# Kernel optimization log

Hardware: AMD Instinct MI355X
Metric: run time of the kernel (lower is better)

Reference implementation:

```python
import jax, jax.numpy as jnp
import numpy as np

B = 8388608  # batch of Euler-angle triples


def _euler_to_vec(angles):
    # angles: [B, 3] = (yaw, pitch, roll)
    # v = R_yaw @ R_pitch @ R_roll @ [0, 0, 1], expanded analytically:
    #   R_roll  @ e_z = [0, -sr, cr]
    #   R_pitch @ ... = [sp*cr, -sr, cp*cr]
    #   R_yaw   @ ... = [cy*sp*cr + sy*sr, sy*sp*cr - cy*sr, cp*cr]
    y, p, r = angles[:, 0], angles[:, 1], angles[:, 2]
    cy, sy = jnp.cos(y), jnp.sin(y)
    cp, sp = jnp.cos(p), jnp.sin(p)
    cr, sr = jnp.cos(r), jnp.sin(r)
    return jnp.stack([cy * sp * cr + sy * sr,
                      sy * sp * cr - cy * sr,
                      cp * cr], axis=-1)  # [B, 3]


def setup_inputs() -> dict:
    key = jax.random.key(0)
    k1, k2 = jax.random.split(key)
    output = jax.random.uniform(k1, (B, 3), dtype=jnp.float32)
    target = jax.random.uniform(k2, (B, 3), dtype=jnp.float32)
    return {"output": output, "target": target}


def reference(output, target):
    two_pi = 2.0 * jnp.pi
    out_ang = two_pi * (output - 0.5)
    tgt_ang = two_pi * (target - 0.5)
    vo = _euler_to_vec(out_ang)  # [B, 3]
    vt = _euler_to_vec(tgt_ang)  # [B, 3]
    cross = jnp.cross(vo, vt)                      # [B, 3]
    cross_norm = jnp.linalg.norm(cross, axis=-1)   # [B]
    dot = jnp.sum(vo * vt, axis=-1)                # [B]
    per_sample = 1.0 - cross_norm + dot
    return jnp.sum(per_sample)
```

## Files before the change

kernel.cpp:

```cpp
#include <hip/hip_runtime.h>
#include <math.h>


#define NBLOCKS 1024
#define NTHREADS 512
#define TILE_ROWS 1024
#define TILE_F2 (TILE_ROWS * 3 / 2)

__device__ __forceinline__ float2 ntload2(const double* p) {
  double d = __builtin_nontemporal_load(p);
  return __builtin_bit_cast(float2, d);
}

__device__ __forceinline__ float sample_loss(float a, float b, float c,
                                             float d, float e, float f) {
  float oy = a - 0.5f, op = b - 0.5f, orr = c - 0.5f;
  float ty = d - 0.5f, tp = e - 0.5f, trr = f - 0.5f;

  float cy = __builtin_amdgcn_cosf(oy), sy = __builtin_amdgcn_sinf(oy);
  float cp = __builtin_amdgcn_cosf(op), sp = __builtin_amdgcn_sinf(op);
  float cr = __builtin_amdgcn_cosf(orr), sr = __builtin_amdgcn_sinf(orr);

  float vox = cy * sp * cr + sy * sr;
  float voy = sy * sp * cr - cy * sr;
  float voz = cp * cr;

  float cy2 = __builtin_amdgcn_cosf(ty), sy2 = __builtin_amdgcn_sinf(ty);
  float cp2 = __builtin_amdgcn_cosf(tp), sp2 = __builtin_amdgcn_sinf(tp);
  float cr2 = __builtin_amdgcn_cosf(trr), sr2 = __builtin_amdgcn_sinf(trr);

  float vtx = cy2 * sp2 * cr2 + sy2 * sr2;
  float vty = sy2 * sp2 * cr2 - cy2 * sr2;
  float vtz = cp2 * cr2;

  float crx = voy * vtz - voz * vty;
  float cry = voz * vtx - vox * vtz;
  float crz = vox * vty - voy * vtx;

  float cn = sqrtf(crx * crx + cry * cry + crz * crz);
  float dot = vox * vtx + voy * vty + voz * vtz;
  return 1.0f - cn + dot;
}

template <int NT>
__device__ __forceinline__ float block_reduce(float acc) {
  #pragma unroll
  for (int off = 32; off > 0; off >>= 1) acc += __shfl_down(acc, off, 64);
  __shared__ float ws[NT / 64];
  int lane = threadIdx.x & 63;
  int wave = threadIdx.x >> 6;
  if (lane == 0) ws[wave] = acc;
  __syncthreads();
  float tot = 0.0f;
  if (threadIdx.x == 0) {
    #pragma unroll
    for (int w = 0; w < NT / 64; ++w) tot += ws[w];
  }
  return tot;
}

__global__ __launch_bounds__(NTHREADS) void loss_partial_kernel(
    const float* __restrict__ out, const float* __restrict__ tgt,
    float* __restrict__ partial, int B) {
  __shared__ float2 ldsO2[TILE_F2];
  __shared__ float2 ldsT2[TILE_F2];
  const float* ldsO = (const float*)ldsO2;
  const float* ldsT = (const float*)ldsT2;

  const double* __restrict__ o2 = (const double*)out;
  const double* __restrict__ t2 = (const double*)tgt;

  const int t = threadIdx.x;
  const int ntiles = B / TILE_ROWS;

  float acc = 0.0f;

  int tile = blockIdx.x;
  float2 a0, a1, a2, b0, b1, b2;
  if (tile < ntiles) {
    const int g = tile * TILE_F2 + t;
    a0 = ntload2(o2 + g); a1 = ntload2(o2 + g + NTHREADS); a2 = ntload2(o2 + g + 2 * NTHREADS);
    b0 = ntload2(t2 + g); b1 = ntload2(t2 + g + NTHREADS); b2 = ntload2(t2 + g + 2 * NTHREADS);
  }

  while (tile < ntiles) {
    ldsO2[t] = a0; ldsO2[t + NTHREADS] = a1; ldsO2[t + 2 * NTHREADS] = a2;
    ldsT2[t] = b0; ldsT2[t + NTHREADS] = b1; ldsT2[t + 2 * NTHREADS] = b2;
    __syncthreads();

    const int next = tile + gridDim.x;
    if (next < ntiles) {
      const int g = next * TILE_F2 + t;
      a0 = ntload2(o2 + g); a1 = ntload2(o2 + g + NTHREADS); a2 = ntload2(o2 + g + 2 * NTHREADS);
      b0 = ntload2(t2 + g); b1 = ntload2(t2 + g + NTHREADS); b2 = ntload2(t2 + g + 2 * NTHREADS);
    }

    #pragma unroll
    for (int k = 0; k < TILE_ROWS / NTHREADS; ++k) {
      const int r = t + k * NTHREADS;
      acc += sample_loss(ldsO[3 * r], ldsO[3 * r + 1], ldsO[3 * r + 2],
                         ldsT[3 * r], ldsT[3 * r + 1], ldsT[3 * r + 2]);
    }
    __syncthreads();
    tile = next;
  }

  const int done = ntiles * TILE_ROWS;
  for (int r = done + blockIdx.x * NTHREADS + t; r < B;
       r += gridDim.x * NTHREADS) {
    acc += sample_loss(out[3 * r], out[3 * r + 1], out[3 * r + 2],
                       tgt[3 * r], tgt[3 * r + 1], tgt[3 * r + 2]);
  }

  float tot = block_reduce<NTHREADS>(acc);
  if (t == 0) partial[blockIdx.x] = tot;
}

__global__ __launch_bounds__(64) void final_reduce_kernel(
    const float* __restrict__ partial, int n, float* __restrict__ out) {
  float acc = 0.0f;
  for (int i = threadIdx.x; i < n; i += 64) acc += partial[i];
  #pragma unroll
  for (int off = 32; off > 0; off >>= 1) acc += __shfl_down(acc, off, 64);
  if (threadIdx.x == 0) out[0] = acc;
}

extern "C" void kernel_launch(void* const* d_in, const int* in_sizes, int n_in,
                              void* d_out, int out_size, void* d_ws, size_t ws_size,
                              hipStream_t stream) {
  const float* d_output = (const float*)d_in[0];
  const float* d_target = (const float*)d_in[1];
  float* partial = (float*)d_ws;
  float* out = (float*)d_out;
  const int B = in_sizes[0] / 3;

  loss_partial_kernel<<<NBLOCKS, NTHREADS, 0, stream>>>(d_output, d_target,
                                                        partial, B);
  final_reduce_kernel<<<1, 64, 0, stream>>>(partial, NBLOCKS, out);
}
```

Measured before the change: 38.59 us.

## Stage tiles via global_load_lds with double-buffered LDS, double grid size

Replaces register-staged nontemporal loads plus LDS stores with direct global-to-LDS loads (12-byte per lane) into a double-buffered shared tile, and doubles the block count. This is meant to remove the register round-trip and the extra LDS write instructions, and to increase memory-level parallelism. The loop relies on the single __syncthreads to order the async LDS writes, with no explicit vmcnt wait, so correctness depends on the compiler inserting waits. LDS use doubles, which may reduce occupancy.

```diff
diff --git a/kernel.cpp b/kernel.cpp
--- a/kernel.cpp
+++ b/kernel.cpp
@@ -2,15 +2,9 @@
 #include <math.h>
 
 
-#define NBLOCKS 1024
+#define NBLOCKS 2048
 #define NTHREADS 512
 #define TILE_ROWS 1024
-#define TILE_F2 (TILE_ROWS * 3 / 2)
-
-__device__ __forceinline__ float2 ntload2(const double* p) {
-  double d = __builtin_nontemporal_load(p);
-  return __builtin_bit_cast(float2, d);
-}
 
 __device__ __forceinline__ float sample_loss(float a, float b, float c,
                                              float d, float e, float f) {
@@ -62,46 +56,52 @@
 __global__ __launch_bounds__(NTHREADS) void loss_partial_kernel(
     const float* __restrict__ out, const float* __restrict__ tgt,
     float* __restrict__ partial, int B) {
-  __shared__ float2 ldsO2[TILE_F2];
-  __shared__ float2 ldsT2[TILE_F2];
-  const float* ldsO = (const float*)ldsO2;
-  const float* ldsT = (const float*)ldsT2;
-
-  const double* __restrict__ o2 = (const double*)out;
-  const double* __restrict__ t2 = (const double*)tgt;
+  __shared__ float bufO[2][TILE_ROWS * 3];
+  __shared__ float bufT[2][TILE_ROWS * 3];
 
   const int t = threadIdx.x;
+  const int w = t >> 6;
+  const int l = t & 63;
   const int ntiles = B / TILE_ROWS;
 
   float acc = 0.0f;
+  int tile = blockIdx.x;
+  int cur = 0;
 
-  int tile = blockIdx.x;
-  float2 a0, a1, a2, b0, b1, b2;
-  if (tile < ntiles) {
-    const int g = tile * TILE_F2 + t;
-    a0 = ntload2(o2 + g); a1 = ntload2(o2 + g + NTHREADS); a2 = ntload2(o2 + g + 2 * NTHREADS);
-    b0 = ntload2(t2 + g); b1 = ntload2(t2 + g + NTHREADS); b2 = ntload2(t2 + g + 2 * NTHREADS);
-  }
+  auto stage = [&](int bi, int tl) {
+    const long rowbase = (long)tl * TILE_ROWS;
+    #pragma unroll
+    for (int k = 0; k < 2; ++k) {
+      const int lrow = k * (NTHREADS) + w * 64;
+      const float* gO = out + (rowbase + lrow + l) * 3;
+      const float* gT = tgt + (rowbase + lrow + l) * 3;
+      float* dO = &bufO[bi][lrow * 3];
+      float* dT = &bufT[bi][lrow * 3];
+      __builtin_amdgcn_global_load_lds(
+          (const __attribute__((address_space(1))) void*)gO,
+          (__attribute__((address_space(3))) void*)dO, 12, 0, 0);
+      __builtin_amdgcn_global_load_lds(
+          (const __attribute__((address_space(1))) void*)gT,
+          (__attribute__((address_space(3))) void*)dT, 12, 0, 0);
+    }
+  };
+
+  if (tile < ntiles) stage(0, tile);
+  __syncthreads();
 
   while (tile < ntiles) {
-    ldsO2[t] = a0; ldsO2[t + NTHREADS] = a1; ldsO2[t + 2 * NTHREADS] = a2;
-    ldsT2[t] = b0; ldsT2[t + NTHREADS] = b1; ldsT2[t + 2 * NTHREADS] = b2;
-    __syncthreads();
-
     const int next = tile + gridDim.x;
-    if (next < ntiles) {
-      const int g = next * TILE_F2 + t;
-      a0 = ntload2(o2 + g); a1 = ntload2(o2 + g + NTHREADS); a2 = ntload2(o2 + g + 2 * NTHREADS);
-      b0 = ntload2(t2 + g); b1 = ntload2(t2 + g + NTHREADS); b2 = ntload2(t2 + g + 2 * NTHREADS);
-    }
+    if (next < ntiles) stage(cur ^ 1, next);
 
     #pragma unroll
-    for (int k = 0; k < TILE_ROWS / NTHREADS; ++k) {
+    for (int k = 0; k < 2; ++k) {
       const int r = t + k * NTHREADS;
-      acc += sample_loss(ldsO[3 * r], ldsO[3 * r + 1], ldsO[3 * r + 2],
-                         ldsT[3 * r], ldsT[3 * r + 1], ldsT[3 * r + 2]);
+      acc += sample_loss(bufO[cur][3 * r], bufO[cur][3 * r + 1],
+                         bufO[cur][3 * r + 2], bufT[cur][3 * r],
+                         bufT[cur][3 * r + 1], bufT[cur][3 * r + 2]);
     }
     __syncthreads();
+    cur ^= 1;
     tile = next;
   }
 
```

Measured after the change: 45.03 us. 1.17x slower.
